# Performance work log

Measured on AMD Instinct MI355X. Metric: run time of the kernel, lower is better.

## Reference

```python
import jax, jax.numpy as jnp
import numpy as np

QMAX = 127.0
QMIN = -128.0


def setup_inputs() -> dict:
    key = jax.random.key(0)
    k1, k2, k3 = jax.random.split(key, 3)
    B, N, D, O = 4, 4096, 2048, 2048
    x = jax.random.normal(k1, (B, N, D), dtype=jnp.float32)
    weight = jax.random.normal(k2, (O, D), dtype=jnp.float32)
    bias = jax.random.normal(k3, (O,), dtype=jnp.float32)
    return {"x": x, "weight": weight, "bias": bias}


def reference(x, weight, bias):
    # --- per-row symmetric int8 quantization of the weight [O, D] ---
    w_max = jnp.clip(jnp.max(jnp.abs(weight), axis=1, keepdims=True), 1e-8, None)
    w_scale = (w_max / QMAX)                     # [O, 1]
    w_q = jnp.clip(jnp.round(weight / w_scale), QMIN, QMAX).astype(jnp.int8)
    w_scale = w_scale.squeeze(1).astype(jnp.float32)  # [O]

    # --- dynamic per-row symmetric int8 quantization of x [B, N, D] ---
    x_max = jnp.max(jnp.abs(x), axis=2, keepdims=True)       # [B, N, 1]
    x_scale = jnp.maximum(x_max / QMAX, 1e-12)               # [B, N, 1]
    x_q = jnp.clip(jnp.round(x / x_scale), QMIN, QMAX).astype(jnp.int8)

    # --- int8 GEMM accumulated in int32: [B,N,D] x [O,D]^T -> [B,N,O] ---
    acc = jnp.einsum("bnd,od->bno", x_q.astype(jnp.int32), w_q.astype(jnp.int32))

    # --- dequantize with per-row activation scale and per-out-channel weight scale ---
    y = acc.astype(jnp.float32) * x_scale.astype(jnp.float32) * w_scale[None, None, :]
    y = y + bias
    return y.astype(x.dtype)
```

## Files before the change

### kernel.cpp

```cpp
#include <hip/hip_runtime.h>
#include <stdint.h>
#include <stddef.h>

typedef int v4i __attribute__((ext_vector_type(4)));

#define GLOAD_LDS16(g, l) __builtin_amdgcn_global_load_lds( \
    (const __attribute__((address_space(1))) void*)(g),     \
    (__attribute__((address_space(3))) void*)(l), 16, 0, 0)

__device__ __forceinline__ int pack4(float4 f, float s) {
    int a = (int)rintf(f.x / s); a = a < -128 ? -128 : (a > 127 ? 127 : a);
    int b = (int)rintf(f.y / s); b = b < -128 ? -128 : (b > 127 ? 127 : b);
    int c = (int)rintf(f.z / s); c = c < -128 ? -128 : (c > 127 ? 127 : c);
    int d = (int)rintf(f.w / s); d = d < -128 ? -128 : (d > 127 ? 127 : d);
    return (a & 255) | ((b & 255) << 8) | ((c & 255) << 16) | ((d & 255) << 24);
}

__global__ __launch_bounds__(256) void quant_rows_2048(
    const float* __restrict__ in, signed char* __restrict__ q,
    float* __restrict__ scales, float floorv)
{
    const int lane = threadIdx.x & 63;
    const int row  = blockIdx.x * 4 + (threadIdx.x >> 6);
    const float* rp = in + (size_t)row * 2048;

    float4 v[8];
#pragma unroll
    for (int j = 0; j < 2; ++j) {
        const float4* p = (const float4*)(rp + j * 1024 + lane * 16);
#pragma unroll
        for (int i = 0; i < 4; ++i) v[j * 4 + i] = p[i];
    }
    float am = 0.0f;
#pragma unroll
    for (int i = 0; i < 8; ++i) {
        am = fmaxf(am, fabsf(v[i].x));
        am = fmaxf(am, fabsf(v[i].y));
        am = fmaxf(am, fabsf(v[i].z));
        am = fmaxf(am, fabsf(v[i].w));
    }
#pragma unroll
    for (int off = 32; off; off >>= 1) am = fmaxf(am, __shfl_xor(am, off));
    const float s = fmaxf(am / 127.0f, floorv);

#pragma unroll
    for (int j = 0; j < 2; ++j) {
        int4 pk;
        pk.x = pack4(v[j * 4 + 0], s);
        pk.y = pack4(v[j * 4 + 1], s);
        pk.z = pack4(v[j * 4 + 2], s);
        pk.w = pack4(v[j * 4 + 3], s);
        *(int4*)(q + (size_t)row * 2048 + j * 1024 + lane * 16) = pk;
    }
    if (lane == 0) scales[row] = s;
}

__global__ __launch_bounds__(512, 2) void gemm_i8_pipe(
    const signed char* __restrict__ xq, const signed char* __restrict__ wq,
    const float* __restrict__ xs, const float* __restrict__ ws,
    const float* __restrict__ bias, float* __restrict__ out, int K)
{
    __shared__ __align__(16) signed char lds[131072];

    const int tid  = threadIdx.x;
    const int lane = tid & 63;
    const int wid  = tid >> 6;
    const int wm   = wid >> 2;
    const int wn   = wid & 3;

    const int nwg  = gridDim.x * gridDim.y;
    int orig = blockIdx.y * gridDim.x + blockIdx.x;
    int swz  = ((nwg & 7) == 0) ? ((orig & 7) * (nwg >> 3) + (orig >> 3)) : orig;
    const int brow = (swz / gridDim.x) * 256;
    const int bcol = (swz % gridDim.x) * 256;

    const int srow = tid >> 2;
    const int gch  = (((tid & 3) ^ ((tid >> 3) & 3)) << 4);
    const int lofs = tid << 4;
    const signed char* gA = xq + (size_t)(brow + srow) * K;
    const signed char* gB = wq + (size_t)(bcol + srow) * K;

#define ST_A(tt, half) GLOAD_LDS16(gA + (size_t)(half) * 128 * K + (size_t)(tt) * 64 + gch, \
                                   lds + ((((tt) & 3) << 14) + ((half) << 13) + lofs))
#define ST_B(tt, half) GLOAD_LDS16(gB + (size_t)(half) * 128 * K + (size_t)(tt) * 64 + gch, \
                                   lds + (65536 + (((tt) & 3) << 14) + ((half) << 13) + lofs))

    const int rl   = lane & 15;
    const int ko   = lane >> 4;
    const int slot = ((ko ^ ((rl >> 1) & 3)) << 4);

#define FRAG_A(buf, r) (*(const v4i*)(lds + (((buf) << 14) + (r) * 64 + slot)))
#define FRAG_B(buf, r) (*(const v4i*)(lds + (65536 + ((buf) << 14) + (r) * 64 + slot)))

    v4i acc[8][4] = {};
    const int ar = wm * 128 + rl;
    const int br = wn * 64 + rl;

#define MFMA8(M0, M1)                                                              \
    do {                                                                           \
        __builtin_amdgcn_s_setprio(1);                                             \
        acc[M0][0] = __builtin_amdgcn_mfma_i32_16x16x64_i8(a0, bc0, acc[M0][0], 0, 0, 0); \
        acc[M0][1] = __builtin_amdgcn_mfma_i32_16x16x64_i8(a0, bc1, acc[M0][1], 0, 0, 0); \
        acc[M0][2] = __builtin_amdgcn_mfma_i32_16x16x64_i8(a0, bc2, acc[M0][2], 0, 0, 0); \
        acc[M0][3] = __builtin_amdgcn_mfma_i32_16x16x64_i8(a0, bc3, acc[M0][3], 0, 0, 0); \
        acc[M1][0] = __builtin_amdgcn_mfma_i32_16x16x64_i8(a1, bc0, acc[M1][0], 0, 0, 0); \
        acc[M1][1] = __builtin_amdgcn_mfma_i32_16x16x64_i8(a1, bc1, acc[M1][1], 0, 0, 0); \
        acc[M1][2] = __builtin_amdgcn_mfma_i32_16x16x64_i8(a1, bc2, acc[M1][2], 0, 0, 0); \
        acc[M1][3] = __builtin_amdgcn_mfma_i32_16x16x64_i8(a1, bc3, acc[M1][3], 0, 0, 0); \
        __builtin_amdgcn_s_setprio(0);                                             \
    } while (0)

#define BAR()   __builtin_amdgcn_s_barrier()
#define LGKM3() do { asm volatile("s_waitcnt lgkmcnt(3)" ::: "memory"); \
                     __builtin_amdgcn_sched_barrier(0); } while (0)

    ST_A(0, 0); ST_A(0, 1); ST_B(0, 0); ST_B(0, 1);
    ST_A(1, 0); ST_A(1, 1); ST_B(1, 0); ST_B(1, 1);
    ST_A(2, 0); ST_A(2, 1); ST_B(2, 0); ST_B(2, 1);
    asm volatile("s_waitcnt vmcnt(4)" ::: "memory");
    BAR();

    v4i bc0 = FRAG_B(0, br);
    v4i bc1 = FRAG_B(0, br + 16);
    v4i bc2 = FRAG_B(0, br + 32);
    v4i bc3 = FRAG_B(0, br + 48);
    v4i a0  = FRAG_A(0, ar);
    v4i a1  = FRAG_A(0, ar + 16);
    v4i bn0, bn1, bn2, bn3, na0, na1;

    const int NT = K >> 6;
    for (int t = 0; t < NT; ++t) {
        const int buf  = t & 3;
        const int nbuf = (t + 1) & 3;
        const bool st  = (t + 3 < NT);
        na0 = FRAG_A(buf, ar + 32); na1 = FRAG_A(buf, ar + 48); bn0 = FRAG_B(nbuf, br);
        if (st) ST_A(t + 3, 0);
        BAR(); LGKM3();
        MFMA8(0, 1);
        BAR();
        a0 = na0; a1 = na1;
        na0 = FRAG_A(buf, ar + 64); na1 = FRAG_A(buf, ar + 80); bn1 = FRAG_B(nbuf, br + 16);
        if (st) ST_A(t + 3, 1);
        BAR(); LGKM3();
        MFMA8(2, 3);
        BAR();
        a0 = na0; a1 = na1;
        na0 = FRAG_A(buf, ar + 96); na1 = FRAG_A(buf, ar + 112); bn2 = FRAG_B(nbuf, br + 32);
        if (st) ST_B(t + 3, 0);
        BAR(); LGKM3();
        MFMA8(4, 5);
        BAR();
        a0 = na0; a1 = na1;
        na0 = FRAG_A(nbuf, ar); na1 = FRAG_A(nbuf, ar + 16); bn3 = FRAG_B(nbuf, br + 48);
        if (st) ST_B(t + 3, 1);
        BAR(); LGKM3();
        MFMA8(6, 7);
        if (t + 4 == NT)      asm volatile("s_waitcnt vmcnt(0)" ::: "memory");
        else if (t + 4 < NT)  asm volatile("s_waitcnt vmcnt(4)" ::: "memory");
        BAR();
        a0 = na0; a1 = na1;
        bc0 = bn0; bc1 = bn1; bc2 = bn2; bc3 = bn3;
    }

    const int rg = lane >> 4;
#pragma unroll
    for (int n = 0; n < 4; ++n) {
        const int col = bcol + wn * 64 + n * 16 + rl;
        const float wsc = ws[col];
        const float bv  = bias[col];
#pragma unroll
        for (int m = 0; m < 8; ++m) {
#pragma unroll
            for (int j = 0; j < 4; ++j) {
                const int row = brow + wm * 128 + m * 16 + rg * 4 + j;
                out[(size_t)row * 2048 + col] =
                    (float)acc[m][n][j] * xs[row] * wsc + bv;
            }
        }
    }
#undef ST_A
#undef ST_B
#undef FRAG_A
#undef FRAG_B
#undef MFMA8
#undef BAR
#undef LGKM3
}

extern "C" void kernel_launch(void* const* d_in, const int* in_sizes, int n_in,
                              void* d_out, int out_size, void* d_ws, size_t ws_size,
                              hipStream_t stream) {
    const float* x    = (const float*)d_in[0];
    const float* w    = (const float*)d_in[1];
    const float* bias = (const float*)d_in[2];
    float* out = (float*)d_out;

    const int D = 2048;
    const int O = in_sizes[2];
    const int M = in_sizes[0] / D;

    char* wsb = (char*)d_ws;
    signed char* xq  = (signed char*)wsb;
    signed char* wqp = (signed char*)(wsb + (size_t)M * D);
    float* xs  = (float*)(wsb + (size_t)M * D + (size_t)O * D);
    float* wsc = (float*)(wsb + (size_t)M * D + (size_t)O * D + (size_t)M * 4);

    quant_rows_2048<<<M / 4, 256, 0, stream>>>(x, xq, xs, 1e-12f);
    quant_rows_2048<<<O / 4, 256, 0, stream>>>(w, wqp, wsc, 1e-8f / 127.0f);

    dim3 grid(O / 256, M / 256);
    gemm_i8_pipe<<<grid, 512, 0, stream>>>(xq, wqp, xs, wsc, bias, out, D);
}
```

Baseline: 135.3 us.

## Restructure GEMM main loop into two 16-MFMA phases without cross-tile fragment prefetch

The int8 GEMM inner loop goes from four phases of 8 MFMAs, which prefetched the next tile's fragments into registers, to two phases of 16 MFMAs that load the current tile's B and A fragments, wait on lgkmcnt(0), then compute. Global-to-LDS issues are grouped in pairs and the vmcnt waits are raised so more tiles stay in flight. This halves the barriers per k-tile and drops the register double-buffering. In exchange, LDS read latency is no longer hidden behind the previous MFMAs.

```diff
diff --git a/kernel.cpp b/kernel.cpp
--- a/kernel.cpp
+++ b/kernel.cpp
@@ -96,70 +96,57 @@
     const int ar = wm * 128 + rl;
     const int br = wn * 64 + rl;
 
-#define MFMA8(M0, M1)                                                              \
-    do {                                                                           \
-        __builtin_amdgcn_s_setprio(1);                                             \
-        acc[M0][0] = __builtin_amdgcn_mfma_i32_16x16x64_i8(a0, bc0, acc[M0][0], 0, 0, 0); \
-        acc[M0][1] = __builtin_amdgcn_mfma_i32_16x16x64_i8(a0, bc1, acc[M0][1], 0, 0, 0); \
-        acc[M0][2] = __builtin_amdgcn_mfma_i32_16x16x64_i8(a0, bc2, acc[M0][2], 0, 0, 0); \
-        acc[M0][3] = __builtin_amdgcn_mfma_i32_16x16x64_i8(a0, bc3, acc[M0][3], 0, 0, 0); \
-        acc[M1][0] = __builtin_amdgcn_mfma_i32_16x16x64_i8(a1, bc0, acc[M1][0], 0, 0, 0); \
-        acc[M1][1] = __builtin_amdgcn_mfma_i32_16x16x64_i8(a1, bc1, acc[M1][1], 0, 0, 0); \
-        acc[M1][2] = __builtin_amdgcn_mfma_i32_16x16x64_i8(a1, bc2, acc[M1][2], 0, 0, 0); \
-        acc[M1][3] = __builtin_amdgcn_mfma_i32_16x16x64_i8(a1, bc3, acc[M1][3], 0, 0, 0); \
-        __builtin_amdgcn_s_setprio(0);                                             \
+#define MFMA16(M0)                                                                      \
+    do {                                                                                \
+        __builtin_amdgcn_s_setprio(1);                                                  \
+        _Pragma("unroll")                                                               \
+        for (int mm = 0; mm < 4; ++mm) {                                                \
+            acc[M0 + mm][0] = __builtin_amdgcn_mfma_i32_16x16x64_i8(af[mm], bc0, acc[M0 + mm][0], 0, 0, 0); \
+            acc[M0 + mm][1] = __builtin_amdgcn_mfma_i32_16x16x64_i8(af[mm], bc1, acc[M0 + mm][1], 0, 0, 0); \
+            acc[M0 + mm][2] = __builtin_amdgcn_mfma_i32_16x16x64_i8(af[mm], bc2, acc[M0 + mm][2], 0, 0, 0); \
+            acc[M0 + mm][3] = __builtin_amdgcn_mfma_i32_16x16x64_i8(af[mm], bc3, acc[M0 + mm][3], 0, 0, 0); \
+        }                                                                               \
+        __builtin_amdgcn_s_setprio(0);                                                  \
     } while (0)
 
 #define BAR()   __builtin_amdgcn_s_barrier()
-#define LGKM3() do { asm volatile("s_waitcnt lgkmcnt(3)" ::: "memory"); \
+#define LGKM0() do { asm volatile("s_waitcnt lgkmcnt(0)" ::: "memory"); \
                      __builtin_amdgcn_sched_barrier(0); } while (0)
 
     ST_A(0, 0); ST_A(0, 1); ST_B(0, 0); ST_B(0, 1);
     ST_A(1, 0); ST_A(1, 1); ST_B(1, 0); ST_B(1, 1);
     ST_A(2, 0); ST_A(2, 1); ST_B(2, 0); ST_B(2, 1);
-    asm volatile("s_waitcnt vmcnt(4)" ::: "memory");
+    asm volatile("s_waitcnt vmcnt(8)" ::: "memory");
     BAR();
-
-    v4i bc0 = FRAG_B(0, br);
-    v4i bc1 = FRAG_B(0, br + 16);
-    v4i bc2 = FRAG_B(0, br + 32);
-    v4i bc3 = FRAG_B(0, br + 48);
-    v4i a0  = FRAG_A(0, ar);
-    v4i a1  = FRAG_A(0, ar + 16);
-    v4i bn0, bn1, bn2, bn3, na0, na1;
 
     const int NT = K >> 6;
     for (int t = 0; t < NT; ++t) {
-        const int buf  = t & 3;
-        const int nbuf = (t + 1) & 3;
-        const bool st  = (t + 3 < NT);
-        na0 = FRAG_A(buf, ar + 32); na1 = FRAG_A(buf, ar + 48); bn0 = FRAG_B(nbuf, br);
-        if (st) ST_A(t + 3, 0);
-        BAR(); LGKM3();
-        MFMA8(0, 1);
+        const int buf = t & 3;
+        const bool st = (t + 3 < NT);
+        v4i af[4];
+        v4i bc0 = FRAG_B(buf, br);
+        v4i bc1 = FRAG_B(buf, br + 16);
+        v4i bc2 = FRAG_B(buf, br + 32);
+        v4i bc3 = FRAG_B(buf, br + 48);
+        af[0] = FRAG_A(buf, ar);
+        af[1] = FRAG_A(buf, ar + 16);
+        af[2] = FRAG_A(buf, ar + 32);
+        af[3] = FRAG_A(buf, ar + 48);
+        if (st) { ST_A(t + 3, 0); ST_A(t + 3, 1); }
+        BAR(); LGKM0();
+        MFMA16(0);
         BAR();
-        a0 = na0; a1 = na1;
-        na0 = FRAG_A(buf, ar + 64); na1 = FRAG_A(buf, ar + 80); bn1 = FRAG_B(nbuf, br + 16);
-        if (st) ST_A(t + 3, 1);
-        BAR(); LGKM3();
-        MFMA8(2, 3);
+        af[0] = FRAG_A(buf, ar + 64);
+        af[1] = FRAG_A(buf, ar + 80);
+        af[2] = FRAG_A(buf, ar + 96);
+        af[3] = FRAG_A(buf, ar + 112);
+        if (st) { ST_B(t + 3, 0); ST_B(t + 3, 1); }
+        BAR(); LGKM0();
+        MFMA16(4);
+        if (t <= NT - 4)      asm volatile("s_waitcnt vmcnt(8)" ::: "memory");
+        else if (t == NT - 3) asm volatile("s_waitcnt vmcnt(4)" ::: "memory");
+        else if (t == NT - 2) asm volatile("s_waitcnt vmcnt(0)" ::: "memory");
         BAR();
-        a0 = na0; a1 = na1;
-        na0 = FRAG_A(buf, ar + 96); na1 = FRAG_A(buf, ar + 112); bn2 = FRAG_B(nbuf, br + 32);
-        if (st) ST_B(t + 3, 0);
-        BAR(); LGKM3();
-        MFMA8(4, 5);
-        BAR();
-        a0 = na0; a1 = na1;
-        na0 = FRAG_A(nbuf, ar); na1 = FRAG_A(nbuf, ar + 16); bn3 = FRAG_B(nbuf, br + 48);
-        if (st) ST_B(t + 3, 1);
-        BAR(); LGKM3();
-        MFMA8(6, 7);
-        if (t + 4 == NT)      asm volatile("s_waitcnt vmcnt(0)" ::: "memory");
-        else if (t + 4 < NT)  asm volatile("s_waitcnt vmcnt(4)" ::: "memory");
-        BAR();
-        a0 = na0; a1 = na1;
-        bc0 = bn0; bc1 = bn1; bc2 = bn2; bc3 = bn3;
     }
 
     const int rg = lane >> 4;
@@ -182,9 +169,9 @@
 #undef ST_B
 #undef FRAG_A
 #undef FRAG_B
-#undef MFMA8
+#undef MFMA16
 #undef BAR
-#undef LGKM3
+#undef LGKM0
 }
 
 extern "C" void kernel_launch(void* const* d_in, const int* in_sizes, int n_in,
```

Result: faster. 129.2 us (-4.5%).
